# Performance work log

Measured on AMD Instinct MI355X. Metric: run time of the kernel, lower is better.

Reference implementation:

```python
import jax, jax.numpy as jnp
import numpy as np

SEQ_LEN = 4096
D_MODEL = 768
N_Q = 8
Q_DIM = D_MODEL // N_Q  # 96
WINDOW = 128


def apply_rope(x, theta):
    # x: [L, d]; standard rotary embedding on even/odd pairs.
    L = x.shape[0]
    pos = jnp.arange(L, dtype=x.dtype)
    ang = pos[:, None] * theta[None, :]              # [L, d/2]
    cos, sin = jnp.cos(ang), jnp.sin(ang)
    x_even, x_odd = x[:, 0::2], x[:, 1::2]
    out_even = x_even * cos - x_odd * sin
    out_odd = x_even * sin + x_odd * cos
    return jnp.stack([out_even, out_odd], axis=-1).reshape(x.shape)


def setup_inputs() -> dict:
    key = jax.random.key(0)
    kx, kw1, kb1, kw2, kb2 = jax.random.split(key, 5)
    s_in = 1.0 / np.sqrt(D_MODEL)
    return {
        "x": jax.random.normal(kx, (SEQ_LEN, D_MODEL), dtype=jnp.float32),
        "Wqkv": jax.random.normal(kw1, (Q_DIM * (N_Q + 2), D_MODEL), dtype=jnp.float32) * s_in,
        "bqkv": jax.random.normal(kb1, (Q_DIM * (N_Q + 2),), dtype=jnp.float32) * s_in,
        "Wout": jax.random.normal(kw2, (D_MODEL, D_MODEL), dtype=jnp.float32) * s_in,
        "bout": jax.random.normal(kb2, (D_MODEL,), dtype=jnp.float32) * s_in,
    }


def reference(x, Wqkv, bqkv, Wout, bout):
    L = x.shape[0]
    qkv = x @ Wqkv.T + bqkv                                   # [L, 10*Q_DIM]
    k = qkv[:, :Q_DIM]                                        # [L, Q_DIM]
    v = qkv[:, Q_DIM:2 * Q_DIM]                               # [L, Q_DIM]
    q = qkv[:, 2 * Q_DIM:].reshape(L, N_Q, Q_DIM)             # [L, H, Q_DIM]

    theta = 1.0 / 10000.0 ** (jnp.arange(0, Q_DIM, 2, dtype=jnp.float32) / Q_DIM)
    q = jax.vmap(lambda h: apply_rope(h, theta), in_axes=1, out_axes=1)(q)
    k = apply_rope(k, theta)

    # Banded causal mask: j <= i and j > i - WINDOW
    i = jnp.arange(L)[:, None]
    j = jnp.arange(L)[None, :]
    mask = (j <= i) & (j > i - WINDOW)                        # [L, L] bool

    # NOTE: source multiplies by sqrt(q_dim) (faithful to original code).
    scores = jnp.sqrt(jnp.float32(Q_DIM)) * jnp.einsum('ihd,jd->hij', q, k)  # [H, L, L]
    scores = jnp.where(mask[None, :, :], scores, -jnp.inf)
    attn = jax.nn.softmax(scores, axis=2)                     # each row has >=1 valid (diag)

    out = jnp.einsum('hij,jd->hid', attn, v)                  # [H, L, Q_DIM]
    out = out.transpose(1, 0, 2).reshape(L, -1)               # [L, D_MODEL]
    return out @ Wout.T + bout
```

## Files before the change

### kernel.cpp

```cpp
#include <hip/hip_runtime.h>

typedef _Float16 f16;
typedef _Float16 half8 __attribute__((ext_vector_type(8)));
typedef _Float16 f16x2 __attribute__((ext_vector_type(2)));
typedef _Float16 f16x4 __attribute__((ext_vector_type(4)));
typedef float    f32x4 __attribute__((ext_vector_type(4)));

#define DM    768
#define QD    96
#define MFMA16(a,b,c) __builtin_amdgcn_mfma_f32_16x16x32_f16(a, b, c, 0, 0, 0)

__device__ __forceinline__ void async_copy16(const f16* g, f16* l) {
  __builtin_amdgcn_global_load_lds((const __attribute__((address_space(1))) void*)g,
                                   (__attribute__((address_space(3))) void*)l,
                                   16, 0, 0);
}

__global__ __launch_bounds__(256) void prep_kernel(const float* __restrict__ x,
                                                   const float* __restrict__ Wqkv,
                                                   const float* __restrict__ bqkv,
                                                   const float* __restrict__ Wout,
                                                   f16* __restrict__ xh,
                                                   f16* __restrict__ w1h,
                                                   f16* __restrict__ w2h,
                                                   float* __restrict__ b1p,
                                                   float* __restrict__ ctab,
                                                   float* __restrict__ stab) {
  const int NW1 = 1024 * 768 / 4;
  const int NW2 = 768 * 768 / 4;
  int b = blockIdx.x;
  if (b < 3072) {
    int idx = b * 256 + threadIdx.x;
    f32x4 v = ((const f32x4*)x)[idx];
    f16x4 o;
    o[0] = (f16)v[0]; o[1] = (f16)v[1]; o[2] = (f16)v[2]; o[3] = (f16)v[3];
    ((f16x4*)xh)[idx] = o;
    return;
  }
  if (b < 4420) {
    int idx = (b - 3072) * 256 + threadIdx.x;
    if (idx < NW1) {
      int r = idx / 192;
      f16x4 o;
      if (r < 960) {
        f32x4 v = ((const f32x4*)Wqkv)[idx];
        o[0] = (f16)v[0]; o[1] = (f16)v[1]; o[2] = (f16)v[2]; o[3] = (f16)v[3];
      } else {
        o[0] = (f16)0.f; o[1] = (f16)0.f; o[2] = (f16)0.f; o[3] = (f16)0.f;
      }
      ((f16x4*)w1h)[idx] = o;
    } else if (idx < NW1 + NW2) {
      int j = idx - NW1;
      f32x4 v = ((const f32x4*)Wout)[j];
      f16x4 o;
      o[0] = (f16)v[0]; o[1] = (f16)v[1]; o[2] = (f16)v[2]; o[3] = (f16)v[3];
      ((f16x4*)w2h)[j] = o;
    } else {
      int j = idx - (NW1 + NW2);
      b1p[j] = (j < 960) ? bqkv[j] : 0.f;
    }
    return;
  }
  int idx = (b - 4420) * 256 + threadIdx.x;
  int pos = idx >> 6, f = idx & 63;
  if (f < 48) {
    float theta = exp2f((float)f * -0.27682734f);
    float s, c;
    sincosf((float)pos * theta, &s, &c);
    ctab[pos * 48 + f] = c;
    stab[pos * 48 + f] = s;
  }
}

#define GEMM_VM6  asm volatile("s_waitcnt vmcnt(6)" ::: "memory")
#define GEMM_VM0  asm volatile("s_waitcnt vmcnt(0)" ::: "memory")
#define GEMM_SB   __builtin_amdgcn_s_barrier()
#define GEMM_SCB  __builtin_amdgcn_sched_barrier(0)

#define GEMM_STAGE(NXT, K0)                                         \
  do {                                                              \
    async_copy16(Ap + (K0),           lA0 + (NXT) * 4096);          \
    async_copy16(Ap + 32 * K + (K0),  lA0 + (NXT) * 4096 + 2048);   \
    async_copy16(Bp + (K0),           lB0 + (NXT) * 8192);          \
    async_copy16(Bp + 32 * K + (K0),  lB0 + (NXT) * 8192 + 2048);   \
    async_copy16(Bp + 64 * K + (K0),  lB0 + (NXT) * 8192 + 4096);   \
    async_copy16(Bp + 96 * K + (K0),  lB0 + (NXT) * 8192 + 6144);   \
  } while (0)

#define GEMM_COMPUTE(BUF)                                                      \
  do {                                                                         \
    half8 a[4][2], b[2][2];                                                    \
    _Pragma("unroll")                                                          \
    for (int m = 0; m < 4; ++m) {                                              \
      int row = m * 16 + fr;                                                   \
      _Pragma("unroll")                                                        \
      for (int kk = 0; kk < 2; ++kk) {                                         \
        int c = (kk << 2) | kg;                                                \
        a[m][kk] = *(const half8*)&As[BUF][row * 64 + ((c ^ (row & 7)) << 3)]; \
      }                                                                        \
    }                                                                          \
    _Pragma("unroll")                                                          \
    for (int n = 0; n < 2; ++n) {                                              \
      int row = w * 32 + n * 16 + fr;                                          \
      _Pragma("unroll")                                                        \
      for (int kk = 0; kk < 2; ++kk) {                                         \
        int c = (kk << 2) | kg;                                                \
        b[n][kk] = *(const half8*)&Bs[BUF][row * 64 + ((c ^ (row & 7)) << 3)]; \
      }                                                                        \
    }                                                                          \
    _Pragma("unroll")                                                          \
    for (int m = 0; m < 4; ++m)                                                \
      _Pragma("unroll")                                                        \
      for (int n = 0; n < 2; ++n) {                                            \
        acc[m][n] = MFMA16(a[m][0], b[n][0], acc[m][n]);                       \
        acc[m][n] = MFMA16(a[m][1], b[n][1], acc[m][n]);                       \
      }                                                                        \
  } while (0)

#define GEMM_PROLOGUE_AND_LOOP                                      \
  __shared__ f16 As[2][64 * 64];                                    \
  __shared__ f16 Bs[2][128 * 64];                                   \
  const int t  = threadIdx.x;                                       \
  const int bm = blockIdx.x * 64;                                   \
  const int bn = blockIdx.y * 128;                                  \
  const int w  = t >> 6, l = t & 63;                                \
  const int fr = l & 15, kg = l >> 4;                               \
  f32x4 acc[4][2] = {};                                             \
  const int srow = t >> 3;                                          \
  const int skc  = ((t & 7) ^ (srow & 7)) << 3;   \
  const f16* Ap = A + (size_t)(bm + srow) * K + skc;                \
  const f16* Bp = B + (size_t)(bn + srow) * K + skc;                \
  f16* lA0 = &As[0][t * 8];                                         \
  f16* lB0 = &Bs[0][t * 8];                                         \
  const int nt = K >> 6;                    \
  GEMM_STAGE(0, 0);                                                 \
  GEMM_STAGE(1, 64);                                                \
  for (int tk = 0; tk < nt; tk += 2) {                              \
    GEMM_VM6; GEMM_SB; GEMM_SCB;                                    \
    GEMM_COMPUTE(0);                                                \
    GEMM_SCB; GEMM_SB;                                              \
    if (tk + 2 < nt) GEMM_STAGE(0, (tk + 2) << 6);                  \
    if (tk + 3 < nt) { GEMM_VM6; } else { GEMM_VM0; }               \
    GEMM_SB; GEMM_SCB;                                              \
    GEMM_COMPUTE(1);                                                \
    GEMM_SCB; GEMM_SB;                                              \
    if (tk + 3 < nt) GEMM_STAGE(1, (tk + 3) << 6);                  \
  }

__global__ __launch_bounds__(256) void gemm_f16_tn(const f16* __restrict__ A,
                                                   const f16* __restrict__ B,
                                                   const float* __restrict__ bias,
                                                   float* __restrict__ C,
                                                   int K, int ldc) {
  GEMM_PROLOGUE_AND_LOOP
  const int r0 = kg * 4;
#pragma unroll
  for (int n = 0; n < 2; ++n) {
    int col = bn + w * 32 + n * 16 + fr;
    float bv = bias[col];
#pragma unroll
    for (int m = 0; m < 4; ++m) {
      int row = bm + m * 16 + r0;
#pragma unroll
      for (int r = 0; r < 4; ++r)
        C[(size_t)(row + r) * ldc + col] = acc[m][n][r] + bv;
    }
  }
}

__global__ __launch_bounds__(256) void gemm_qkv_rope(const f16* __restrict__ A,
                                                     const f16* __restrict__ B,
                                                     const float* __restrict__ bias,
                                                     const float* __restrict__ ctab,
                                                     const float* __restrict__ stab,
                                                     f16* __restrict__ qh,
                                                     f16* __restrict__ ql,
                                                     f16* __restrict__ kh,
                                                     f16* __restrict__ kl,
                                                     f16* __restrict__ vT) {
  const int K = 768;
  GEMM_PROLOGUE_AND_LOOP
  const int r0 = kg * 4;
  f16* ls = &As[0][0];
  const int vlo = (bn < 96) ? 96 : bn;
  const int vhi = (bn + 128 < 192) ? (bn + 128) : 192;
  const bool has_v = vlo < vhi;
  if (has_v) __syncthreads();
#pragma unroll
  for (int n = 0; n < 2; ++n) {
    int col = bn + w * 32 + n * 16 + fr;
    float bv = bias[col];
    int seg = (col * 683) >> 16;
    int segoff = col - seg * 96;
    int f = segoff >> 1;
    bool odd = col & 1;
#pragma unroll
    for (int m = 0; m < 4; ++m) {
      int row = bm + m * 16 + r0;
      if (seg == 1) {
        f16x4 pk;
#pragma unroll
        for (int r = 0; r < 4; ++r) pk[r] = (f16)(acc[m][n][r] + bv);
        *(f16x4*)&ls[(col - vlo) * 72 + m * 16 + r0] = pk;
        continue;
      }
#pragma unroll
      for (int r = 0; r < 4; ++r) {
        float v = acc[m][n][r] + bv;
        float p = __shfl_xor(v, 1);
        if (col < 960) {
          float c = ctab[(row + r) * 48 + f];
          float s = stab[(row + r) * 48 + f];
          float e = odd ? p : v;
          float o = odd ? v : p;
          float res = odd ? (e * s + o * c) : (e * c - o * s);
          f16 hi = (f16)res;
          f16 lo = (f16)(res - (float)hi);
          if (seg == 0) {
            kh[(size_t)(row + r) * QD + col] = hi;
            kl[(size_t)(row + r) * QD + col] = lo;
          } else {
            int qc = col - 192;
            qh[(size_t)(row + r) * DM + qc] = hi;
            ql[(size_t)(row + r) * DM + qc] = lo;
          }
        }
      }
    }
  }
  if (has_v) {
    __syncthreads();
    const int nv = vhi - vlo;
    for (int it = 0; it < (nv >> 5); ++it) {
      int idx = t + 256 * it;
      int cl = idx >> 3, sg = idx & 7;
      *(half8*)(vT + (size_t)(vlo - 96 + cl) * 4096 + bm + sg * 8) =
          *(half8*)&ls[cl * 72 + sg * 8];
    }
  }
}

__global__ __launch_bounds__(256) void attn2_kernel(const f16* __restrict__ qh,
                                                    const f16* __restrict__ ql,
                                                    const f16* __restrict__ kh,
                                                    const f16* __restrict__ kl,
                                                    const f16* __restrict__ vT,
                                                    f16* __restrict__ aout) {
  __shared__ f16 kbuf[192 * 104];
  __shared__ f16 klbuf[192 * 104];
  __shared__ f16 vbuf[96 * 200];
  __shared__ f16 pbuf[4][32 * 40];
  const int t  = threadIdx.x, w = t >> 6, l = t & 63;
  const int fr = l & 15, kg = l >> 4;
  const int i0 = blockIdx.x * 64;
  const int h  = blockIdx.y * 2 + (w >> 1);
  const int q0 = (w & 1) * 32;
  const int jbase = i0 - 128;
  const int nlo = (w & 1) ? 2 : 0;

  for (int it = 0; it < 9; ++it) {
    int c = t + 256 * it;
    int row = c / 12, seg = c - row * 12;
    int jabs = jbase + row; if (jabs < 0) jabs = 0;
    *(half8*)(kbuf + row * 104 + seg * 8) =
        *(const half8*)(kh + (size_t)jabs * QD + seg * 8);
    *(half8*)(klbuf + row * 104 + seg * 8) =
        *(const half8*)(kl + (size_t)jabs * QD + seg * 8);
  }
  for (int it = 0; it < 9; ++it) {
    int c = t + 256 * it;
    int row = c / 24, seg = c - row * 24;
    int col0 = jbase + seg * 8; if (col0 < 0) col0 = 0;
    *(half8*)(vbuf + row * 200 + seg * 8) =
        *(const half8*)(vT + (size_t)row * 4096 + col0);
  }

  half8 a_h[2][3], a_l[2][3];
#pragma unroll
  for (int m = 0; m < 2; ++m) {
    size_t qoff = (size_t)(i0 + q0 + m * 16 + fr) * DM + h * QD;
#pragma unroll
    for (int kc = 0; kc < 3; ++kc) {
      a_h[m][kc] = *(const half8*)(qh + qoff + kc * 32 + kg * 8);
      a_l[m][kc] = *(const half8*)(ql + qoff + kc * 32 + kg * 8);
    }
  }
  __syncthreads();

  f32x4 s[2][12];
#pragma unroll
  for (int m = 0; m < 2; ++m)
#pragma unroll
    for (int n = 0; n < 12; ++n)
      s[m][n] = (f32x4){0.f, 0.f, 0.f, 0.f};

  __builtin_amdgcn_s_setprio(1);
#pragma unroll
  for (int n = 0; n < 12; ++n) {
    if (n < nlo || n >= nlo + 10) continue;
    int krow = n * 16 + fr;
#pragma unroll
    for (int kc = 0; kc < 3; ++kc) {
      half8 b_h = *(const half8*)(kbuf + krow * 104 + kc * 32 + kg * 8);
      half8 b_l = *(const half8*)(klbuf + krow * 104 + kc * 32 + kg * 8);
      s[0][n] = MFMA16(a_h[0][kc], b_h, s[0][n]);
      s[1][n] = MFMA16(a_h[1][kc], b_h, s[1][n]);
      s[0][n] = MFMA16(a_l[0][kc], b_h, s[0][n]);
      s[1][n] = MFMA16(a_l[1][kc], b_h, s[1][n]);
      s[0][n] = MFMA16(a_h[0][kc], b_l, s[0][n]);
      s[1][n] = MFMA16(a_h[1][kc], b_l, s[1][n]);
    }
  }
  __builtin_amdgcn_s_setprio(0);

  const int jmin = (i0 < 128) ? (128 - i0) : 0;
  const float scale = 9.79795897113271f;
  float mx[2][4], sm[2][4], inv[2][4];
#pragma unroll
  for (int m = 0; m < 2; ++m)
#pragma unroll
    for (int r = 0; r < 4; ++r) mx[m][r] = -1e30f;

#pragma unroll
  for (int m = 0; m < 2; ++m)
#pragma unroll
    for (int n = 0; n < 12; ++n) {
      if (n < nlo || n >= nlo + 10) continue;
      int jloc = n * 16 + fr;
#pragma unroll
      for (int r = 0; r < 4; ++r) {
        int iloc = q0 + m * 16 + kg * 4 + r;
        bool valid = (jloc > iloc) && (jloc <= iloc + 128) && (jloc >= jmin);
        float v = valid ? s[m][n][r] * scale : -1e30f;
        s[m][n][r] = v;
        mx[m][r] = fmaxf(mx[m][r], v);
      }
    }
#pragma unroll
  for (int m = 0; m < 2; ++m)
#pragma unroll
    for (int r = 0; r < 4; ++r) {
      float v = mx[m][r];
      v = fmaxf(v, __shfl_xor(v, 1));
      v = fmaxf(v, __shfl_xor(v, 2));
      v = fmaxf(v, __shfl_xor(v, 4));
      v = fmaxf(v, __shfl_xor(v, 8));
      mx[m][r] = v;
      sm[m][r] = 0.f;
    }
#pragma unroll
  for (int m = 0; m < 2; ++m)
#pragma unroll
    for (int n = 0; n < 12; ++n) {
      if (n < nlo || n >= nlo + 10) continue;
#pragma unroll
      for (int r = 0; r < 4; ++r) {
        float p = __expf(s[m][n][r] - mx[m][r]);
        s[m][n][r] = p;
        sm[m][r] += p;
      }
    }
#pragma unroll
  for (int m = 0; m < 2; ++m)
#pragma unroll
    for (int r = 0; r < 4; ++r) {
      float v = sm[m][r];
      v += __shfl_xor(v, 1);
      v += __shfl_xor(v, 2);
      v += __shfl_xor(v, 4);
      v += __shfl_xor(v, 8);
      inv[m][r] = 1.f / v;
    }

  f16* pw = pbuf[w];
  const int c6lo = nlo >> 1;
  f32x4 o[2][6];
#pragma unroll
  for (int m = 0; m < 2; ++m)
#pragma unroll
    for (int dn = 0; dn < 6; ++dn)
      o[m][dn] = (f32x4){0.f, 0.f, 0.f, 0.f};

#pragma unroll
  for (int c6 = 0; c6 < 6; ++c6) {
    if (c6 < c6lo || c6 >= c6lo + 5) continue;
#pragma unroll
    for (int m = 0; m < 2; ++m)
#pragma unroll
      for (int nn = 0; nn < 2; ++nn)
#pragma unroll
        for (int r = 0; r < 4; ++r)
          pw[(m * 16 + kg * 4 + r) * 40 + nn * 16 + fr] = (f16)s[m][2 * c6 + nn][r];
    half8 ap0 = *(half8*)(pw + fr * 40 + kg * 8);
    half8 ap1 = *(half8*)(pw + (16 + fr) * 40 + kg * 8);
    __builtin_amdgcn_s_setprio(1);
#pragma unroll
    for (int dn = 0; dn < 6; ++dn) {
      half8 bv = *(half8*)(vbuf + (dn * 16 + fr) * 200 + c6 * 32 + kg * 8);
      o[0][dn] = MFMA16(ap0, bv, o[0][dn]);
      o[1][dn] = MFMA16(ap1, bv, o[1][dn]);
    }
    __builtin_amdgcn_s_setprio(0);
  }

#pragma unroll
  for (int m = 0; m < 2; ++m)
#pragma unroll
    for (int dn = 0; dn < 6; ++dn) {
      int col = h * QD + dn * 16 + fr;
#pragma unroll
      for (int r = 0; r < 4; ++r) {
        int row = i0 + q0 + m * 16 + kg * 4 + r;
        aout[(size_t)row * DM + col] = (f16)(o[m][dn][r] * inv[m][r]);
      }
    }
}

extern "C" void kernel_launch(void* const* d_in, const int* in_sizes, int n_in,
                              void* d_out, int out_size, void* d_ws, size_t ws_size,
                              hipStream_t stream) {
  const float* x    = (const float*)d_in[0];
  const float* Wqkv = (const float*)d_in[1];
  const float* bqkv = (const float*)d_in[2];
  const float* Wout = (const float*)d_in[3];
  const float* bout = (const float*)d_in[4];
  float* out = (float*)d_out;

  char* ws = (char*)d_ws;
  f16*   xh   = (f16*)(ws);
  f16*   w1h  = (f16*)(ws + 6291456);
  f16*   w2h  = (f16*)(ws + 7864320);
  float* b1p  = (float*)(ws + 9043968);
  float* ctab = (float*)(ws + 9048064);
  float* stab = (float*)(ws + 9834496);
  f16*   qh   = (f16*)(ws + 10620928);
  f16*   ql   = (f16*)(ws + 16912384);
  f16*   kh   = (f16*)(ws + 23203840);
  f16*   kl   = (f16*)(ws + 23990272);
  f16*   vT   = (f16*)(ws + 24776704);
  f16*   aout = (f16*)(ws + 25563136);

  prep_kernel<<<dim3(5444), dim3(256), 0, stream>>>(x, Wqkv, bqkv, Wout,
                                                    xh, w1h, w2h, b1p, ctab, stab);
  gemm_qkv_rope<<<dim3(64, 8), dim3(256), 0, stream>>>(xh, w1h, b1p, ctab, stab,
                                                       qh, ql, kh, kl, vT);
  attn2_kernel<<<dim3(64, 4), dim3(256), 0, stream>>>(qh, ql, kh, kl, vT, aout);
  gemm_f16_tn<<<dim3(64, 6), dim3(256), 0, stream>>>(aout, w2h, bout, out, 768, 768);
}
```

Measured before the change: 56.91 us.

## Switch GEMMs to single-wave 64x64 tiles with barrier-free pipelining

New measurement: 66.25 us. 1.16x slower.

```diff
diff --git a/kernel.cpp b/kernel.cpp
--- a/kernel.cpp
+++ b/kernel.cpp
@@ -72,24 +72,23 @@
   }
 }
 
-#define GEMM_VM6  asm volatile("s_waitcnt vmcnt(6)" ::: "memory")
-#define GEMM_VM0  asm volatile("s_waitcnt vmcnt(0)" ::: "memory")
-#define GEMM_SB   __builtin_amdgcn_s_barrier()
-#define GEMM_SCB  __builtin_amdgcn_sched_barrier(0)
-
-#define GEMM_STAGE(NXT, K0)                                         \
-  do {                                                              \
-    async_copy16(Ap + (K0),           lA0 + (NXT) * 4096);          \
-    async_copy16(Ap + 32 * K + (K0),  lA0 + (NXT) * 4096 + 2048);   \
-    async_copy16(Bp + (K0),           lB0 + (NXT) * 8192);          \
-    async_copy16(Bp + 32 * K + (K0),  lB0 + (NXT) * 8192 + 2048);   \
-    async_copy16(Bp + 64 * K + (K0),  lB0 + (NXT) * 8192 + 4096);   \
-    async_copy16(Bp + 96 * K + (K0),  lB0 + (NXT) * 8192 + 6144);   \
+#define SGEMM_VMC16 asm volatile("s_waitcnt vmcnt(16)" ::: "memory")
+#define SGEMM_VMC0  asm volatile("s_waitcnt vmcnt(0)"  ::: "memory")
+#define SCB __builtin_amdgcn_sched_barrier(0)
+
+#define SGEMM_STAGE(BUF, K0)                                             \
+  do {                                                                   \
+    _Pragma("unroll")                                                    \
+    for (int i = 0; i < 8; ++i)                                          \
+      async_copy16(Ap + (size_t)i * 8 * K + (K0), lA + (BUF) * 4096 + i * 512); \
+    _Pragma("unroll")                                                    \
+    for (int i = 0; i < 8; ++i)                                          \
+      async_copy16(Bp + (size_t)i * 8 * K + (K0), lB + (BUF) * 4096 + i * 512); \
   } while (0)
 
-#define GEMM_COMPUTE(BUF)                                                      \
+#define SGEMM_COMPUTE(BUF)                                                     \
   do {                                                                         \
-    half8 a[4][2], b[2][2];                                                    \
+    half8 a[4][2], b[4][2];                                                    \
     _Pragma("unroll")                                                          \
     for (int m = 0; m < 4; ++m) {                                              \
       int row = m * 16 + fr;                                                   \
@@ -97,66 +96,53 @@
       for (int kk = 0; kk < 2; ++kk) {                                         \
         int c = (kk << 2) | kg;                                                \
         a[m][kk] = *(const half8*)&As[BUF][row * 64 + ((c ^ (row & 7)) << 3)]; \
-      }                                                                        \
-    }                                                                          \
-    _Pragma("unroll")                                                          \
-    for (int n = 0; n < 2; ++n) {                                              \
-      int row = w * 32 + n * 16 + fr;                                          \
-      _Pragma("unroll")                                                        \
-      for (int kk = 0; kk < 2; ++kk) {                                         \
-        int c = (kk << 2) | kg;                                                \
-        b[n][kk] = *(const half8*)&Bs[BUF][row * 64 + ((c ^ (row & 7)) << 3)]; \
+        b[m][kk] = *(const half8*)&Bs[BUF][row * 64 + ((c ^ (row & 7)) << 3)]; \
       }                                                                        \
     }                                                                          \
     _Pragma("unroll")                                                          \
     for (int m = 0; m < 4; ++m)                                                \
       _Pragma("unroll")                                                        \
-      for (int n = 0; n < 2; ++n) {                                            \
+      for (int n = 0; n < 4; ++n) {                                            \
         acc[m][n] = MFMA16(a[m][0], b[n][0], acc[m][n]);                       \
         acc[m][n] = MFMA16(a[m][1], b[n][1], acc[m][n]);                       \
       }                                                                        \
   } while (0)
 
-#define GEMM_PROLOGUE_AND_LOOP                                      \
+#define SGEMM_PROLOGUE_AND_LOOP                                     \
   __shared__ f16 As[2][64 * 64];                                    \
-  __shared__ f16 Bs[2][128 * 64];                                   \
-  const int t  = threadIdx.x;                                       \
+  __shared__ f16 Bs[2][64 * 64];                                    \
+  const int l  = threadIdx.x;                                       \
   const int bm = blockIdx.x * 64;                                   \
-  const int bn = blockIdx.y * 128;                                  \
-  const int w  = t >> 6, l = t & 63;                                \
+  const int bn = blockIdx.y * 64;                                   \
   const int fr = l & 15, kg = l >> 4;                               \
-  f32x4 acc[4][2] = {};                                             \
-  const int srow = t >> 3;                                          \
-  const int skc  = ((t & 7) ^ (srow & 7)) << 3;   \
+  f32x4 acc[4][4] = {};                                             \
+  const int srow = l >> 3;                                          \
+  const int skc  = ((l & 7) ^ (srow & 7)) << 3;                     \
   const f16* Ap = A + (size_t)(bm + srow) * K + skc;                \
   const f16* Bp = B + (size_t)(bn + srow) * K + skc;                \
-  f16* lA0 = &As[0][t * 8];                                         \
-  f16* lB0 = &Bs[0][t * 8];                                         \
-  const int nt = K >> 6;                    \
-  GEMM_STAGE(0, 0);                                                 \
-  GEMM_STAGE(1, 64);                                                \
-  for (int tk = 0; tk < nt; tk += 2) {                              \
-    GEMM_VM6; GEMM_SB; GEMM_SCB;                                    \
-    GEMM_COMPUTE(0);                                                \
-    GEMM_SCB; GEMM_SB;                                              \
-    if (tk + 2 < nt) GEMM_STAGE(0, (tk + 2) << 6);                  \
-    if (tk + 3 < nt) { GEMM_VM6; } else { GEMM_VM0; }               \
-    GEMM_SB; GEMM_SCB;                                              \
-    GEMM_COMPUTE(1);                                                \
-    GEMM_SCB; GEMM_SB;                                              \
-    if (tk + 3 < nt) GEMM_STAGE(1, (tk + 3) << 6);                  \
-  }
-
-__global__ __launch_bounds__(256) void gemm_f16_tn(const f16* __restrict__ A,
-                                                   const f16* __restrict__ B,
-                                                   const float* __restrict__ bias,
-                                                   float* __restrict__ C,
-                                                   int K, int ldc) {
-  GEMM_PROLOGUE_AND_LOOP
+  f16* lA = &As[0][l * 8];                                          \
+  f16* lB = &Bs[0][l * 8];                                          \
+  const int nt = K >> 6;                            \
+  SGEMM_STAGE(0, 0);                                                \
+  SGEMM_STAGE(1, 64);                                               \
+  for (int tk = 0; tk < nt; ++tk) {                                 \
+    if (tk + 1 < nt) { SGEMM_VMC16; } else { SGEMM_VMC0; }          \
+    SCB;                                                            \
+    SGEMM_COMPUTE(tk & 1);                                          \
+    SCB;                                                            \
+    if (tk + 2 < nt) SGEMM_STAGE(tk & 1, (tk + 2) << 6);            \
+  }
+
+__global__ __launch_bounds__(64) void gemm_f16_tn(const f16* __restrict__ A,
+                                                  const f16* __restrict__ B,
+                                                  const float* __restrict__ bias,
+                                                  float* __restrict__ C,
+                                                  int K, int ldc) {
+  SGEMM_PROLOGUE_AND_LOOP
   const int r0 = kg * 4;
 #pragma unroll
-  for (int n = 0; n < 2; ++n) {
-    int col = bn + w * 32 + n * 16 + fr;
+  for (int n = 0; n < 4; ++n) {
+    int col = bn + n * 16 + fr;
     float bv = bias[col];
 #pragma unroll
     for (int m = 0; m < 4; ++m) {
@@ -168,32 +154,31 @@
   }
 }
 
-__global__ __launch_bounds__(256) void gemm_qkv_rope(const f16* __restrict__ A,
-                                                     const f16* __restrict__ B,
-                                                     const float* __restrict__ bias,
-                                                     const float* __restrict__ ctab,
-                                                     const float* __restrict__ stab,
-                                                     f16* __restrict__ qh,
-                                                     f16* __restrict__ ql,
-                                                     f16* __restrict__ kh,
-                                                     f16* __restrict__ kl,
-                                                     f16* __restrict__ vT) {
+__global__ __launch_bounds__(64) void gemm_qkv_rope(const f16* __restrict__ A,
+                                                    const f16* __restrict__ B,
+                                                    const float* __restrict__ bias,
+                                                    const float* __restrict__ ctab,
+                                                    const float* __restrict__ stab,
+                                                    f16* __restrict__ qh,
+                                                    f16* __restrict__ ql,
+                                                    f16* __restrict__ kh,
+                                                    f16* __restrict__ kl,
+                                                    f16* __restrict__ vT) {
   const int K = 768;
-  GEMM_PROLOGUE_AND_LOOP
+  SGEMM_PROLOGUE_AND_LOOP
   const int r0 = kg * 4;
   f16* ls = &As[0][0];
   const int vlo = (bn < 96) ? 96 : bn;
-  const int vhi = (bn + 128 < 192) ? (bn + 128) : 192;
+  const int vhi = (bn + 64 < 192) ? (bn + 64) : 192;
   const bool has_v = vlo < vhi;
-  if (has_v) __syncthreads();
-#pragma unroll
-  for (int n = 0; n < 2; ++n) {
-    int col = bn + w * 32 + n * 16 + fr;
+  const bool even = !(fr & 1);
+#pragma unroll
+  for (int n = 0; n < 4; ++n) {
+    int col = bn + n * 16 + fr;
     float bv = bias[col];
     int seg = (col * 683) >> 16;
     int segoff = col - seg * 96;
     int f = segoff >> 1;
-    bool odd = col & 1;
 #pragma unroll
     for (int m = 0; m < 4; ++m) {
       int row = bm + m * 16 + r0;
@@ -208,31 +193,29 @@
       for (int r = 0; r < 4; ++r) {
         float v = acc[m][n][r] + bv;
         float p = __shfl_xor(v, 1);
-        if (col < 960) {
+        if (even) {
           float c = ctab[(row + r) * 48 + f];
           float s = stab[(row + r) * 48 + f];
-          float e = odd ? p : v;
-          float o = odd ? v : p;
-          float res = odd ? (e * s + o * c) : (e * c - o * s);
-          f16 hi = (f16)res;
-          f16 lo = (f16)(res - (float)hi);
+          float re = v * c - p * s;
+          float ro = v * s + p * c;
+          f16 hie = (f16)re, hio = (f16)ro;
+          f16x2 hv; hv[0] = hie; hv[1] = hio;
+          f16x2 lv; lv[0] = (f16)(re - (float)hie); lv[1] = (f16)(ro - (float)hio);
           if (seg == 0) {
-            kh[(size_t)(row + r) * QD + col] = hi;
-            kl[(size_t)(row + r) * QD + col] = lo;
+            *(f16x2*)(kh + (size_t)(row + r) * QD + col) = hv;
+            *(f16x2*)(kl + (size_t)(row + r) * QD + col) = lv;
           } else {
             int qc = col - 192;
-            qh[(size_t)(row + r) * DM + qc] = hi;
-            ql[(size_t)(row + r) * DM + qc] = lo;
+            *(f16x2*)(qh + (size_t)(row + r) * DM + qc) = hv;
+            *(f16x2*)(ql + (size_t)(row + r) * DM + qc) = lv;
           }
         }
       }
     }
   }
   if (has_v) {
-    __syncthreads();
     const int nv = vhi - vlo;
-    for (int it = 0; it < (nv >> 5); ++it) {
-      int idx = t + 256 * it;
+    for (int idx = l; idx < nv * 8; idx += 64) {
       int cl = idx >> 3, sg = idx & 7;
       *(half8*)(vT + (size_t)(vlo - 96 + cl) * 4096 + bm + sg * 8) =
           *(half8*)&ls[cl * 72 + sg * 8];
@@ -442,8 +425,8 @@
 
   prep_kernel<<<dim3(5444), dim3(256), 0, stream>>>(x, Wqkv, bqkv, Wout,
                                                     xh, w1h, w2h, b1p, ctab, stab);
-  gemm_qkv_rope<<<dim3(64, 8), dim3(256), 0, stream>>>(xh, w1h, b1p, ctab, stab,
+  gemm_qkv_rope<<<dim3(64, 15), dim3(64), 0, stream>>>(xh, w1h, b1p, ctab, stab,
                                                        qh, ql, kh, kl, vT);
   attn2_kernel<<<dim3(64, 4), dim3(256), 0, stream>>>(qh, ql, kh, kl, vT, aout);
-  gemm_f16_tn<<<dim3(64, 6), dim3(256), 0, stream>>>(aout, w2h, bout, out, 768, 768);
-}
+  gemm_f16_tn<<<dim3(64, 12), dim3(64), 0, stream>>>(aout, w2h, bout, out, 768, 768);
+}
```

## Halve GEMM M-tile to 32 rows, simplify pipeline, and pair RoPE stores

Applied to the files above, without the earlier changes.

New measurement: 54.92 us. -3.5%, faster.

```diff
diff --git a/kernel.cpp b/kernel.cpp
--- a/kernel.cpp
+++ b/kernel.cpp
@@ -72,26 +72,25 @@
   }
 }
 
-#define GEMM_VM6  asm volatile("s_waitcnt vmcnt(6)" ::: "memory")
+#define GEMM_VM5  asm volatile("s_waitcnt vmcnt(5)" ::: "memory")
 #define GEMM_VM0  asm volatile("s_waitcnt vmcnt(0)" ::: "memory")
 #define GEMM_SB   __builtin_amdgcn_s_barrier()
 #define GEMM_SCB  __builtin_amdgcn_sched_barrier(0)
 
-#define GEMM_STAGE(NXT, K0)                                         \
+#define GEMM_STAGE(BUF, K0)                                         \
   do {                                                              \
-    async_copy16(Ap + (K0),           lA0 + (NXT) * 4096);          \
-    async_copy16(Ap + 32 * K + (K0),  lA0 + (NXT) * 4096 + 2048);   \
-    async_copy16(Bp + (K0),           lB0 + (NXT) * 8192);          \
-    async_copy16(Bp + 32 * K + (K0),  lB0 + (NXT) * 8192 + 2048);   \
-    async_copy16(Bp + 64 * K + (K0),  lB0 + (NXT) * 8192 + 4096);   \
-    async_copy16(Bp + 96 * K + (K0),  lB0 + (NXT) * 8192 + 6144);   \
+    async_copy16(Ap + (K0),           lA0 + (BUF) * 2048);          \
+    async_copy16(Bp + (K0),           lB0 + (BUF) * 8192);          \
+    async_copy16(Bp + 32 * K + (K0),  lB0 + (BUF) * 8192 + 2048);   \
+    async_copy16(Bp + 64 * K + (K0),  lB0 + (BUF) * 8192 + 4096);   \
+    async_copy16(Bp + 96 * K + (K0),  lB0 + (BUF) * 8192 + 6144);   \
   } while (0)
 
 #define GEMM_COMPUTE(BUF)                                                      \
   do {                                                                         \
-    half8 a[4][2], b[2][2];                                                    \
+    half8 a[2][2], b[2][2];                                                    \
     _Pragma("unroll")                                                          \
-    for (int m = 0; m < 4; ++m) {                                              \
+    for (int m = 0; m < 2; ++m) {                                              \
       int row = m * 16 + fr;                                                   \
       _Pragma("unroll")                                                        \
       for (int kk = 0; kk < 2; ++kk) {                                         \
@@ -109,7 +108,7 @@
       }                                                                        \
     }                                                                          \
     _Pragma("unroll")                                                          \
-    for (int m = 0; m < 4; ++m)                                                \
+    for (int m = 0; m < 2; ++m)                                                \
       _Pragma("unroll")                                                        \
       for (int n = 0; n < 2; ++n) {                                            \
         acc[m][n] = MFMA16(a[m][0], b[n][0], acc[m][n]);                       \
@@ -118,33 +117,29 @@
   } while (0)
 
 #define GEMM_PROLOGUE_AND_LOOP                                      \
-  __shared__ f16 As[2][64 * 64];                                    \
+  __shared__ f16 As[2][32 * 64];                                    \
   __shared__ f16 Bs[2][128 * 64];                                   \
   const int t  = threadIdx.x;                                       \
-  const int bm = blockIdx.x * 64;                                   \
+  const int bm = blockIdx.x * 32;                                   \
   const int bn = blockIdx.y * 128;                                  \
   const int w  = t >> 6, l = t & 63;                                \
   const int fr = l & 15, kg = l >> 4;                               \
-  f32x4 acc[4][2] = {};                                             \
+  f32x4 acc[2][2] = {};                                             \
   const int srow = t >> 3;                                          \
   const int skc  = ((t & 7) ^ (srow & 7)) << 3;   \
   const f16* Ap = A + (size_t)(bm + srow) * K + skc;                \
   const f16* Bp = B + (size_t)(bn + srow) * K + skc;                \
   f16* lA0 = &As[0][t * 8];                                         \
   f16* lB0 = &Bs[0][t * 8];                                         \
-  const int nt = K >> 6;                    \
+  const int nt = K >> 6;                                  \
   GEMM_STAGE(0, 0);                                                 \
   GEMM_STAGE(1, 64);                                                \
-  for (int tk = 0; tk < nt; tk += 2) {                              \
-    GEMM_VM6; GEMM_SB; GEMM_SCB;                                    \
-    GEMM_COMPUTE(0);                                                \
+  for (int tk = 0; tk < nt; ++tk) {                                 \
+    if (tk + 1 < nt) { GEMM_VM5; } else { GEMM_VM0; }               \
+    GEMM_SB; GEMM_SCB;                                              \
+    GEMM_COMPUTE(tk & 1);                                           \
     GEMM_SCB; GEMM_SB;                                              \
-    if (tk + 2 < nt) GEMM_STAGE(0, (tk + 2) << 6);                  \
-    if (tk + 3 < nt) { GEMM_VM6; } else { GEMM_VM0; }               \
-    GEMM_SB; GEMM_SCB;                                              \
-    GEMM_COMPUTE(1);                                                \
-    GEMM_SCB; GEMM_SB;                                              \
-    if (tk + 3 < nt) GEMM_STAGE(1, (tk + 3) << 6);                  \
+    if (tk + 2 < nt) GEMM_STAGE(tk & 1, (tk + 2) << 6);             \
   }
 
 __global__ __launch_bounds__(256) void gemm_f16_tn(const f16* __restrict__ A,
@@ -159,7 +154,7 @@
     int col = bn + w * 32 + n * 16 + fr;
     float bv = bias[col];
 #pragma unroll
-    for (int m = 0; m < 4; ++m) {
+    for (int m = 0; m < 2; ++m) {
       int row = bm + m * 16 + r0;
 #pragma unroll
       for (int r = 0; r < 4; ++r)
@@ -185,44 +180,42 @@
   const int vlo = (bn < 96) ? 96 : bn;
   const int vhi = (bn + 128 < 192) ? (bn + 128) : 192;
   const bool has_v = vlo < vhi;
-  if (has_v) __syncthreads();
+  const bool even = !(fr & 1);
 #pragma unroll
   for (int n = 0; n < 2; ++n) {
     int col = bn + w * 32 + n * 16 + fr;
     float bv = bias[col];
     int seg = (col * 683) >> 16;
-    int segoff = col - seg * 96;
-    int f = segoff >> 1;
-    bool odd = col & 1;
-#pragma unroll
-    for (int m = 0; m < 4; ++m) {
+    int f = (col - seg * 96) >> 1;
+#pragma unroll
+    for (int m = 0; m < 2; ++m) {
       int row = bm + m * 16 + r0;
       if (seg == 1) {
         f16x4 pk;
 #pragma unroll
         for (int r = 0; r < 4; ++r) pk[r] = (f16)(acc[m][n][r] + bv);
-        *(f16x4*)&ls[(col - vlo) * 72 + m * 16 + r0] = pk;
+        *(f16x4*)&ls[(col - vlo) * 40 + m * 16 + r0] = pk;
         continue;
       }
 #pragma unroll
       for (int r = 0; r < 4; ++r) {
         float v = acc[m][n][r] + bv;
         float p = __shfl_xor(v, 1);
-        if (col < 960) {
+        if (even && col < 960) {
           float c = ctab[(row + r) * 48 + f];
           float s = stab[(row + r) * 48 + f];
-          float e = odd ? p : v;
-          float o = odd ? v : p;
-          float res = odd ? (e * s + o * c) : (e * c - o * s);
-          f16 hi = (f16)res;
-          f16 lo = (f16)(res - (float)hi);
+          float re = v * c - p * s;
+          float ro = v * s + p * c;
+          f16 hie = (f16)re, hio = (f16)ro;
+          f16x2 hv; hv[0] = hie; hv[1] = hio;
+          f16x2 lv; lv[0] = (f16)(re - (float)hie); lv[1] = (f16)(ro - (float)hio);
           if (seg == 0) {
-            kh[(size_t)(row + r) * QD + col] = hi;
-            kl[(size_t)(row + r) * QD + col] = lo;
+            *(f16x2*)(kh + (size_t)(row + r) * QD + col) = hv;
+            *(f16x2*)(kl + (size_t)(row + r) * QD + col) = lv;
           } else {
             int qc = col - 192;
-            qh[(size_t)(row + r) * DM + qc] = hi;
-            ql[(size_t)(row + r) * DM + qc] = lo;
+            *(f16x2*)(qh + (size_t)(row + r) * DM + qc) = hv;
+            *(f16x2*)(ql + (size_t)(row + r) * DM + qc) = lv;
           }
         }
       }
@@ -231,11 +224,10 @@
   if (has_v) {
     __syncthreads();
     const int nv = vhi - vlo;
-    for (int it = 0; it < (nv >> 5); ++it) {
-      int idx = t + 256 * it;
-      int cl = idx >> 3, sg = idx & 7;
+    for (int idx = t; idx < nv * 4; idx += 256) {
+      int cl = idx >> 2, sg = idx & 3;
       *(half8*)(vT + (size_t)(vlo - 96 + cl) * 4096 + bm + sg * 8) =
-          *(half8*)&ls[cl * 72 + sg * 8];
+          *(half8*)&ls[cl * 40 + sg * 8];
     }
   }
 }
@@ -442,8 +434,8 @@
 
   prep_kernel<<<dim3(5444), dim3(256), 0, stream>>>(x, Wqkv, bqkv, Wout,
                                                     xh, w1h, w2h, b1p, ctab, stab);
-  gemm_qkv_rope<<<dim3(64, 8), dim3(256), 0, stream>>>(xh, w1h, b1p, ctab, stab,
-                                                       qh, ql, kh, kl, vT);
+  gemm_qkv_rope<<<dim3(128, 8), dim3(256), 0, stream>>>(xh, w1h, b1p, ctab, stab,
+                                                        qh, ql, kh, kl, vT);
   attn2_kernel<<<dim3(64, 4), dim3(256), 0, stream>>>(qh, ql, kh, kl, vT, aout);
-  gemm_f16_tn<<<dim3(64, 6), dim3(256), 0, stream>>>(aout, w2h, bout, out, 768, 768);
-}
+  gemm_f16_tn<<<dim3(128, 6), dim3(256), 0, stream>>>(aout, w2h, bout, out, 768, 768);
+}
```
